# Kernel optimization log

Measured on AMD Instinct MI355X. Metric: run time of the kernel, lower is better.

## Reference

```python
import jax, jax.numpy as jnp
import numpy as np

B, T, D = 64, 512, 768
H1, H2, OUT = 512, 512, 256

def _masked_lstm(x, lengths, Wih, Whh, b):
    # x: [B,T,Din] -> (outs [B,T,H], final hidden [B,H]). torch gate order: i,f,g,o.
    Bm, Tm, _ = x.shape
    H = Whh.shape[1]
    x_proj = jnp.einsum('btd,gd->btg', x, Wih) + b          # [B,T,4H], input proj hoisted out of scan
    mask = jnp.arange(Tm)[None, :] < lengths[:, None]        # [B,T]
    def step(carry, inp):
        h, c = carry
        xg, m = inp
        gates = xg + h @ Whh.T
        i, f, g, o = jnp.split(gates, 4, axis=-1)
        c_new = jax.nn.sigmoid(f) * c + jax.nn.sigmoid(i) * jnp.tanh(g)
        h_new = jax.nn.sigmoid(o) * jnp.tanh(c_new)
        m = m[:, None]
        h = jnp.where(m, h_new, h)      # hold state past seq end (pack_padded semantics)
        c = jnp.where(m, c_new, c)
        return (h, c), jnp.where(m, h_new, 0.0)  # pad_packed zero-fills
    h0 = jnp.zeros((Bm, H), x.dtype)
    (hT, _), outs = jax.lax.scan(step, (h0, h0), (x_proj.transpose(1, 0, 2), mask.T))
    return outs.transpose(1, 0, 2), hT

def _reverse_valid(x, lengths):
    # reverse each row within its valid length; zeros beyond (packed-sequence reversal)
    Tm = x.shape[1]
    idx = lengths[:, None] - 1 - jnp.arange(Tm)[None, :]
    valid = idx >= 0
    xr = jnp.take_along_axis(x, jnp.clip(idx, 0, Tm - 1)[..., None], axis=1)
    return jnp.where(valid[..., None], xr, 0.0)

def _bilstm_sum(x, lengths, Wih_f, Whh_f, b_f, Wih_b, Whh_b, b_b):
    out_f, h_f = _masked_lstm(x, lengths, Wih_f, Whh_f, b_f)
    out_b_rev, h_b = _masked_lstm(_reverse_valid(x, lengths), lengths, Wih_b, Whh_b, b_b)
    return out_f + _reverse_valid(out_b_rev, lengths), h_f, h_b

def _forward(x, W1f_ih, W1f_hh, b1f, W1b_ih, W1b_hh, b1b,
             W2f_ih, W2f_hh, b2f, W2b_ih, W2b_hh, b2b, W3, b3):
    lengths = jnp.sum(x[:, :, 0] != 0, axis=1)               # pad_with = 0
    out1, _, _ = _bilstm_sum(x, lengths, W1f_ih, W1f_hh, b1f, W1b_ih, W1b_hh, b1b)
    # direction sum already done inside _bilstm_sum; dropout is identity at eval
    _, h2f, h2b = _bilstm_sum(out1, lengths, W2f_ih, W2f_hh, b2f, W2b_ih, W2b_hh, b2b)
    h = h2f + h2b                                             # out_h[-2] (fwd) + out_h[-1] (bwd)
    return h @ W3.T + b3

def setup_inputs() -> dict:
    key = jax.random.key(0)
    ks = jax.random.split(key, 16)
    lengths = jax.random.randint(ks[0], (B,), T // 2, T + 1)
    x = jax.random.normal(ks[1], (B, T, D), dtype=jnp.float32)
    x = x * (jnp.arange(T)[None, :] < lengths[:, None])[..., None].astype(jnp.float32)
    def w(k, shape, fan):
        return jax.random.uniform(k, shape, jnp.float32, -1.0, 1.0) / np.sqrt(fan).astype(np.float32)
    return {
        'x': x,
        'W1f_ih': w(ks[2], (4 * H1, D), H1), 'W1f_hh': w(ks[3], (4 * H1, H1), H1), 'b1f': w(ks[4], (4 * H1,), H1),
        'W1b_ih': w(ks[5], (4 * H1, D), H1), 'W1b_hh': w(ks[6], (4 * H1, H1), H1), 'b1b': w(ks[7], (4 * H1,), H1),
        'W2f_ih': w(ks[8], (4 * H2, H1), H2), 'W2f_hh': w(ks[9], (4 * H2, H2), H2), 'b2f': w(ks[10], (4 * H2,), H2),
        'W2b_ih': w(ks[11], (4 * H2, H1), H2), 'W2b_hh': w(ks[12], (4 * H2, H2), H2), 'b2b': w(ks[13], (4 * H2,), H2),
        'W3': w(ks[14], (OUT, H2), H2), 'b3': w(ks[15], (OUT,), H2),
    }

def reference(x, W1f_ih, W1f_hh, b1f, W1b_ih, W1b_hh, b1b,
              W2f_ih, W2f_hh, b2f, W2b_ih, W2b_hh, b2b, W3, b3):
    return _forward(x, W1f_ih, W1f_hh, b1f, W1b_ih, W1b_hh, b1b,
                    W2f_ih, W2f_hh, b2f, W2b_ih, W2b_hh, b2b, W3, b3)
```

## Files before the change

kernel.cpp:

```cpp
#include <hip/hip_runtime.h>


#define WS_B 64
#define WS_T 512
#define WS_D 768
#define WS_H 512
#define NTOK 32768

typedef unsigned short u16;
typedef unsigned int u32;
typedef __attribute__((ext_vector_type(8))) short short8;
typedef __attribute__((ext_vector_type(4))) float f32x4;

__device__ __forceinline__ float bf2f(u16 u) {
    u32 x = ((u32)u) << 16;
    return __builtin_bit_cast(float, x);
}
__device__ __forceinline__ u16 f2bf(float f) {
    u32 x = __builtin_bit_cast(u32, f);
    u32 r = (x + 0x7FFFu + ((x >> 16) & 1u)) >> 16;
    return (u16)r;
}
__device__ __forceinline__ float sigf(float x) {
    return __builtin_amdgcn_rcpf(1.0f + __builtin_amdgcn_exp2f(-1.4426950408889634f * x));
}
__device__ __forceinline__ float tanh_f(float x) {
    return 2.0f * __builtin_amdgcn_rcpf(1.0f + __builtin_amdgcn_exp2f(-2.8853900817779268f * x)) - 1.0f;
}
__device__ __forceinline__ void cstore_u16(u16* p, u16 v) {
    __hip_atomic_store(p, v, __ATOMIC_RELAXED, __HIP_MEMORY_SCOPE_AGENT);
}

__global__ void lengths_kernel(const float* __restrict__ x, int* __restrict__ len) {
    int b = blockIdx.x;
    float v = x[((size_t)b * WS_T + threadIdx.x) * WS_D];
    unsigned long long m = __ballot(v != 0.0f);
    __shared__ int part[8];
    if ((threadIdx.x & 63) == 0) part[threadIdx.x >> 6] = __popcll(m);
    __syncthreads();
    if (threadIdx.x == 0) {
        int s = 0;
        for (int i = 0; i < 8; ++i) s += part[i];
        len[b] = s;
    }
}

__global__ void cvt_kernel(const float* __restrict__ s, u16* __restrict__ d, int n4) {
    int i = blockIdx.x * 256 + threadIdx.x;
    if (i >= n4) return;
    float4 v = ((const float4*)s)[i];
    ushort4 r;
    r.x = f2bf(v.x); r.y = f2bf(v.y); r.z = f2bf(v.z); r.w = f2bf(v.w);
    ((ushort4*)d)[i] = r;
}

__global__ void add_bf16_kernel(u16* __restrict__ a, const u16* __restrict__ b, int n8) {
    int i = blockIdx.x * 256 + threadIdx.x;
    if (i >= n8) return;
    ushort4 va0 = ((const ushort4*)a)[2 * i], va1 = ((const ushort4*)a)[2 * i + 1];
    ushort4 vb0 = ((const ushort4*)b)[2 * i], vb1 = ((const ushort4*)b)[2 * i + 1];
    ushort4 r0, r1;
    r0.x = f2bf(bf2f(va0.x) + bf2f(vb0.x)); r0.y = f2bf(bf2f(va0.y) + bf2f(vb0.y));
    r0.z = f2bf(bf2f(va0.z) + bf2f(vb0.z)); r0.w = f2bf(bf2f(va0.w) + bf2f(vb0.w));
    r1.x = f2bf(bf2f(va1.x) + bf2f(vb1.x)); r1.y = f2bf(bf2f(va1.y) + bf2f(vb1.y));
    r1.z = f2bf(bf2f(va1.z) + bf2f(vb1.z)); r1.w = f2bf(bf2f(va1.w) + bf2f(vb1.w));
    ((ushort4*)a)[2 * i] = r0; ((ushort4*)a)[2 * i + 1] = r1;
}

#define BM 128
#define BN 128
#define BKT 64
template <int A32>
__global__ __launch_bounds__(256) void gemm_bt(
    const void* __restrict__ Av, const u16* __restrict__ W,
    const float* __restrict__ bias, _Float16* __restrict__ C,
    int M, int N, int K)
{
    __shared__ u16 As[BM * BKT];
    __shared__ u16 Bs[BN * BKT];
    const int tid = threadIdx.x;
    const int lane = tid & 63, w = tid >> 6;
    const int ntiles = N / BN;
    const int mt = blockIdx.x / ntiles, nt = blockIdx.x - mt * ntiles;
    const int m0 = mt * BM, n0 = nt * BN;
    const int wr = (w >> 1) * 64, wc = (w & 1) * 64;
    const int kin = (lane >> 4) << 4;
    f32x4 acc[4][4] = {};
    for (int k0 = 0; k0 < K; k0 += BKT) {
#pragma unroll
        for (int it = 0; it < 4; ++it) {
            int off = it * 4096 + tid * 16;
            int row = off >> 7;
            int ce = (off & 127) >> 1;
            const u16* gb = W + (size_t)(n0 + row) * K + (k0 + ce);
            char* lb = (char*)Bs + it * 4096 + w * 1024;
            __builtin_amdgcn_global_load_lds(
                (const __attribute__((address_space(1))) u32*)gb,
                (__attribute__((address_space(3))) u32*)lb, 16, 0, 0);
            if constexpr (A32) {
                const float* ga = (const float*)Av + (size_t)(m0 + row) * K + (k0 + ce);
                float4 v0 = ((const float4*)ga)[0];
                float4 v1 = ((const float4*)ga)[1];
                u32 p0 = ((u32)f2bf(v0.y) << 16) | f2bf(v0.x);
                u32 p1 = ((u32)f2bf(v0.w) << 16) | f2bf(v0.z);
                u32 p2 = ((u32)f2bf(v1.y) << 16) | f2bf(v1.x);
                u32 p3 = ((u32)f2bf(v1.w) << 16) | f2bf(v1.z);
                *(uint4*)((char*)As + off) = make_uint4(p0, p1, p2, p3);
            } else {
                const u16* ga = (const u16*)Av + (size_t)(m0 + row) * K + (k0 + ce);
                char* la = (char*)As + it * 4096 + w * 1024;
                __builtin_amdgcn_global_load_lds(
                    (const __attribute__((address_space(1))) u32*)ga,
                    (__attribute__((address_space(3))) u32*)la, 16, 0, 0);
            }
        }
        asm volatile("s_waitcnt vmcnt(0)" ::: "memory");
        __syncthreads();
#pragma unroll
        for (int ks = 0; ks < 2; ++ks) {
            short8 av[4], bv[4];
#pragma unroll
            for (int mi = 0; mi < 4; ++mi)
                av[mi] = *(const short8*)((const char*)As + (wr + mi * 16 + (lane & 15)) * 128 + ks * 64 + kin);
#pragma unroll
            for (int ni = 0; ni < 4; ++ni)
                bv[ni] = *(const short8*)((const char*)Bs + (wc + ni * 16 + (lane & 15)) * 128 + ks * 64 + kin);
#pragma unroll
            for (int mi = 0; mi < 4; ++mi)
#pragma unroll
                for (int ni = 0; ni < 4; ++ni)
                    acc[mi][ni] = __builtin_amdgcn_mfma_f32_16x16x32_bf16(av[mi], bv[ni], acc[mi][ni], 0, 0, 0);
        }
        __syncthreads();
    }
    const int crow0 = m0 + wr + ((lane >> 4) << 2);
    const int ccol0 = n0 + wc + (lane & 15);
#pragma unroll
    for (int ni = 0; ni < 4; ++ni) {
        float bs = bias[ccol0 + ni * 16];
#pragma unroll
        for (int mi = 0; mi < 4; ++mi)
#pragma unroll
            for (int e = 0; e < 4; ++e)
                C[(size_t)(crow0 + mi * 16 + e) * N + (ccol0 + ni * 16)] =
                    (_Float16)(acc[mi][ni][e] + bs);
    }
}

__global__ __launch_bounds__(256, 1) void lstm_rec(
    const u16* __restrict__ whhF, const u16* __restrict__ whhB,
    const _Float16* __restrict__ xgF, const _Float16* __restrict__ xgB,
    const int* __restrict__ lengths,
    u16* __restrict__ hb,
    float* __restrict__ hfin,
    u16* __restrict__ outF, u16* __restrict__ outB,
    int* __restrict__ flags,
    int writeOut, int dir0)
{
    __shared__ __align__(16) char wlds[65536];
    const int tid = threadIdx.x;
    const int lane = tid & 63, w = tid >> 6;
    const int grp = blockIdx.x >> 5, wgl = blockIdx.x & 31;
    const int dir = dir0 + grp;
    const int hb_col = wgl << 4;
    const u16* whh = dir ? whhB : whhF;
    const _Float16* xg = dir ? xgB : xgF;
    u16* outp = dir ? outB : outF;
    int* myflags = flags + (grp << 5);
    const int colL = lane & 15;
    const int hcol = hb_col + colL;
    const int qw = lane >> 4;
    const int arow = (w << 4) + colL;
    const int kofs = qw << 3;

#pragma unroll
    for (int j = 0; j < 16; ++j) {
        int f = (w << 4) + j, kk = f >> 2, g = f & 3;
        int R = (g << 9) + hb_col + colL;
        uint4 v = *(const uint4*)(whh + (size_t)R * WS_H + kk * 32 + kofs);
        *(uint4*)(wlds + f * 1024 + lane * 16) = v;
    }
    int mylen[4], myb[4];
#pragma unroll
    for (int e = 0; e < 4; ++e) {
        myb[e] = (w << 4) + (qw << 2) + e;
        mylen[e] = lengths[myb[e]];
    }
    float hreg[4] = {0.f, 0.f, 0.f, 0.f}, creg[4] = {0.f, 0.f, 0.f, 0.f};
    float xq[4][4];

#pragma unroll
    for (int e = 0; e < 4; ++e) {
        int len = mylen[e];
        int tx = dir ? (len - 1) : 0;
        int txc = tx < 0 ? 0 : (tx > 511 ? 511 : tx);
        const _Float16* xr = xg + ((size_t)(myb[e] * WS_T + txc) << 11);
        xq[e][0] = (float)xr[hcol];
        xq[e][1] = (float)xr[512 + hcol];
        xq[e][2] = (float)xr[1024 + hcol];
        xq[e][3] = (float)xr[1536 + hcol];
    }
    __syncthreads();

    for (int s = 0; s < WS_T; ++s) {
        const int pr = s & 1;
        const u16* hg = hb + (dir * 2 + pr) * 32768;
        u16* hw = hb + (dir * 2 + (pr ^ 1)) * 32768;

        short8 av[16];
#pragma unroll
        for (int kk = 0; kk < 16; ++kk)
            av[kk] = *(const short8*)(hg + arow * WS_H + kk * 32 + kofs);
        f32x4 acc[4] = {};
#pragma unroll
        for (int kk = 0; kk < 16; ++kk) {
            const char* wp = wlds + (kk << 12) + lane * 16;
#pragma unroll
            for (int g = 0; g < 4; ++g) {
                short8 bg = *(const short8*)(wp + (g << 10));
                acc[g] = __builtin_amdgcn_mfma_f32_16x16x32_bf16(av[kk], bg, acc[g], 0, 0, 0);
            }
        }

#pragma unroll
        for (int e = 0; e < 4; ++e) {
            if (s < mylen[e]) {
                float gi = acc[0][e] + xq[e][0];
                float gf = acc[1][e] + xq[e][1];
                float gg = acc[2][e] + xq[e][2];
                float go = acc[3][e] + xq[e][3];
                float cn = sigf(gf) * creg[e] + sigf(gi) * tanh_f(gg);
                creg[e] = cn;
                hreg[e] = sigf(go) * tanh_f(cn);
            }
            cstore_u16(hw + myb[e] * WS_H + hcol, f2bf(hreg[e]));
        }
        __syncthreads();
        if (tid == 0)
            __hip_atomic_store(&myflags[wgl], s + 1, __ATOMIC_RELAXED, __HIP_MEMORY_SCOPE_AGENT);

        if (writeOut) {
#pragma unroll
            for (int e = 0; e < 4; ++e) {
                int len = mylen[e];
                int tx = dir ? (len - 1 - s) : s;
                if (s < len)
                    outp[((size_t)(myb[e] * WS_T + tx)) * 512 + hcol] = f2bf(hreg[e]);
            }
        }
        if (s == WS_T - 1) {
#pragma unroll
            for (int e = 0; e < 4; ++e)
                hfin[dir * 32768 + myb[e] * WS_H + hcol] = hreg[e];
        }
        if (s < WS_T - 1) {
#pragma unroll
            for (int e = 0; e < 4; ++e) {
                int len = mylen[e];
                int tx = dir ? (len - 2 - s) : (s + 1);
                int txc = tx < 0 ? 0 : (tx > 511 ? 511 : tx);
                const _Float16* xr = xg + ((size_t)(myb[e] * WS_T + txc) << 11);
                xq[e][0] = (float)xr[hcol];
                xq[e][1] = (float)xr[512 + hcol];
                xq[e][2] = (float)xr[1024 + hcol];
                xq[e][3] = (float)xr[1536 + hcol];
            }
            if (tid < 32) {
                while (__hip_atomic_load(&myflags[tid], __ATOMIC_RELAXED, __HIP_MEMORY_SCOPE_AGENT) <= s)
                    __builtin_amdgcn_s_sleep(1);
            }
            __syncthreads();
            if (tid == 0) {
                int v = __hip_atomic_load(&myflags[0], __ATOMIC_ACQUIRE, __HIP_MEMORY_SCOPE_AGENT);
                asm volatile("" :: "v"(v));
            }
            __syncthreads();
        }
    }
}

__global__ void final_kernel(const float* __restrict__ hf, const float* __restrict__ hbk,
                             const float* __restrict__ W3, const float* __restrict__ b3,
                             float* __restrict__ out) {
    int b = blockIdx.x, o = threadIdx.x;
    __shared__ float h2[512];
    for (int k = threadIdx.x; k < 512; k += 256) h2[k] = hf[b * 512 + k] + hbk[b * 512 + k];
    __syncthreads();
    float s = b3[o];
#pragma unroll 8
    for (int k = 0; k < 512; ++k) s += h2[k] * W3[o * 512 + k];
    out[b * 256 + o] = s;
}

#define MB(x) ((size_t)(x) << 20)

extern "C" void kernel_launch(void* const* d_in, const int* in_sizes, int n_in,
                              void* d_out, int out_size, void* d_ws, size_t ws_size,
                              hipStream_t stream) {
    (void)in_sizes; (void)n_in; (void)out_size;
    const float* x      = (const float*)d_in[0];
    const float* b1f    = (const float*)d_in[3];
    const float* b1b    = (const float*)d_in[6];
    const float* b2f    = (const float*)d_in[9];
    const float* b2b    = (const float*)d_in[12];
    const float* W3     = (const float*)d_in[13];
    const float* b3     = (const float*)d_in[14];
    float* out = (float*)d_out;
    char* ws = (char*)d_ws;

    enum : size_t {
        O_LEN  = 0,
        O_FLG  = 512,
        O_HB1  = 4096,
        O_HB2  = O_HB1 + 262144,
        O_HF1  = O_HB2 + 262144,
        O_HF2  = O_HF1 + 262144,
        O_CTRL_END = O_HF2 + 262144
    };
    const size_t O_W1FH = MB(2),  O_W1BH = MB(4),  O_W2FH = MB(6),  O_W2BH = MB(8);
    const size_t O_W1FI = MB(10), O_W1BI = MB(13), O_W2FI = MB(16), O_W2BI = MB(18);
    const size_t O_OUTF = MB(20), O_OUTB = MB(52);
    const size_t O_XG0  = MB(84), O_XG1  = MB(212);
    const size_t NEED_SEQ = MB(212), NEED_PAR = MB(340);
    if (ws_size < NEED_SEQ) return;
    const bool par = ws_size >= NEED_PAR;

    (void)hipMemsetAsync(ws, 0, O_CTRL_END, stream);
    (void)hipMemsetAsync(ws + O_OUTF, 0, MB(64), stream);

    int* lenp = (int*)(ws + O_LEN);
    lengths_kernel<<<64, 512, 0, stream>>>(x, lenp);

    cvt_kernel<<<1024, 256, 0, stream>>>((const float*)d_in[2],  (u16*)(ws + O_W1FH), 262144);
    cvt_kernel<<<1024, 256, 0, stream>>>((const float*)d_in[5],  (u16*)(ws + O_W1BH), 262144);
    cvt_kernel<<<1024, 256, 0, stream>>>((const float*)d_in[8],  (u16*)(ws + O_W2FH), 262144);
    cvt_kernel<<<1024, 256, 0, stream>>>((const float*)d_in[11], (u16*)(ws + O_W2BH), 262144);
    cvt_kernel<<<1536, 256, 0, stream>>>((const float*)d_in[1],  (u16*)(ws + O_W1FI), 393216);
    cvt_kernel<<<1536, 256, 0, stream>>>((const float*)d_in[4],  (u16*)(ws + O_W1BI), 393216);
    cvt_kernel<<<1024, 256, 0, stream>>>((const float*)d_in[7],  (u16*)(ws + O_W2FI), 262144);
    cvt_kernel<<<1024, 256, 0, stream>>>((const float*)d_in[10], (u16*)(ws + O_W2BI), 262144);

    _Float16* xg0 = (_Float16*)(ws + O_XG0);
    _Float16* xg1 = par ? (_Float16*)(ws + O_XG1) : xg0;
    u16* outFp = (u16*)(ws + O_OUTF);
    u16* outBp = (u16*)(ws + O_OUTB);

    if (par) {
        gemm_bt<1><<<4096, 256, 0, stream>>>(x, (u16*)(ws + O_W1FI), b1f, xg0, NTOK, 2048, 768);
        gemm_bt<1><<<4096, 256, 0, stream>>>(x, (u16*)(ws + O_W1BI), b1b, xg1, NTOK, 2048, 768);
        lstm_rec<<<64, 256, 0, stream>>>((u16*)(ws + O_W1FH), (u16*)(ws + O_W1BH),
                                         xg0, xg1, lenp,
                                         (u16*)(ws + O_HB1), (float*)(ws + O_HF1),
                                         outFp, outBp, (int*)(ws + O_FLG), 1, 0);
        add_bf16_kernel<<<8192, 256, 0, stream>>>(outFp, outBp, 2097152);
        gemm_bt<0><<<4096, 256, 0, stream>>>(outFp, (u16*)(ws + O_W2FI), b2f, xg0, NTOK, 2048, 512);
        gemm_bt<0><<<4096, 256, 0, stream>>>(outFp, (u16*)(ws + O_W2BI), b2b, xg1, NTOK, 2048, 512);
        lstm_rec<<<64, 256, 0, stream>>>((u16*)(ws + O_W2FH), (u16*)(ws + O_W2BH),
                                         xg0, xg1, lenp,
                                         (u16*)(ws + O_HB2), (float*)(ws + O_HF2),
                                         outFp, outBp, (int*)(ws + O_FLG + 512), 0, 0);
    } else {
        gemm_bt<1><<<4096, 256, 0, stream>>>(x, (u16*)(ws + O_W1FI), b1f, xg0, NTOK, 2048, 768);
        lstm_rec<<<32, 256, 0, stream>>>((u16*)(ws + O_W1FH), (u16*)(ws + O_W1FH),
                                         xg0, xg0, lenp,
                                         (u16*)(ws + O_HB1), (float*)(ws + O_HF1),
                                         outFp, outBp, (int*)(ws + O_FLG), 1, 0);
        gemm_bt<1><<<4096, 256, 0, stream>>>(x, (u16*)(ws + O_W1BI), b1b, xg0, NTOK, 2048, 768);
        lstm_rec<<<32, 256, 0, stream>>>((u16*)(ws + O_W1BH), (u16*)(ws + O_W1BH),
                                         xg0, xg0, lenp,
                                         (u16*)(ws + O_HB1), (float*)(ws + O_HF1),
                                         outFp, outBp, (int*)(ws + O_FLG + 256), 1, 1);
        add_bf16_kernel<<<8192, 256, 0, stream>>>(outFp, outBp, 2097152);
        gemm_bt<0><<<4096, 256, 0, stream>>>(outFp, (u16*)(ws + O_W2FI), b2f, xg0, NTOK, 2048, 512);
        lstm_rec<<<32, 256, 0, stream>>>((u16*)(ws + O_W2FH), (u16*)(ws + O_W2FH),
                                         xg0, xg0, lenp,
                                         (u16*)(ws + O_HB2), (float*)(ws + O_HF2),
                                         outFp, outBp, (int*)(ws + O_FLG + 512), 0, 0);
        gemm_bt<0><<<4096, 256, 0, stream>>>(outFp, (u16*)(ws + O_W2BI), b2b, xg0, NTOK, 2048, 512);
        lstm_rec<<<32, 256, 0, stream>>>((u16*)(ws + O_W2BH), (u16*)(ws + O_W2BH),
                                         xg0, xg0, lenp,
                                         (u16*)(ws + O_HB2), (float*)(ws + O_HF2),
                                         outFp, outBp, (int*)(ws + O_FLG + 768), 0, 1);
    }
    final_kernel<<<64, 256, 0, stream>>>((const float*)(ws + O_HF2),
                                         (const float*)(ws + O_HF2) + 32768, W3, b3, out);
}
```

Baseline: 5.946 ms.

## Move inter-workgroup wait before h load and defer xq/output work past MFMA

Restructures the recurrent LSTM step loop: the spin-wait on peer workgroup flags moves to the top of each step, and the sleep is dropped in favour of a tight spin with an acquire fence. The next-step input projection loads and the previous step's output stores are issued right after the hidden-state loads, ahead of the MFMA chain, so their latency overlaps the matmul. The flag store becomes a release store, and one of the two extra __syncthreads per step is removed. The risk is more spin pressure on memory and reliance on correct release/acquire ordering between workgroups.

```diff
diff --git a/kernel.cpp b/kernel.cpp
--- a/kernel.cpp
+++ b/kernel.cpp
@@ -187,7 +187,7 @@
         mylen[e] = lengths[myb[e]];
     }
     float hreg[4] = {0.f, 0.f, 0.f, 0.f}, creg[4] = {0.f, 0.f, 0.f, 0.f};
-    float xq[4][4];
+    float xq[4][4], xqn[4][4];
 
 #pragma unroll
     for (int e = 0; e < 4; ++e) {
@@ -207,10 +207,45 @@
         const u16* hg = hb + (dir * 2 + pr) * 32768;
         u16* hw = hb + (dir * 2 + (pr ^ 1)) * 32768;
 
+        if (s) {
+            if (tid < 32) {
+                while (__hip_atomic_load(&myflags[tid], __ATOMIC_RELAXED,
+                                         __HIP_MEMORY_SCOPE_AGENT) < s) {}
+            }
+            __syncthreads();
+            __builtin_amdgcn_fence(__ATOMIC_ACQUIRE, "agent");
+        }
+
         short8 av[16];
 #pragma unroll
         for (int kk = 0; kk < 16; ++kk)
             av[kk] = *(const short8*)(hg + arow * WS_H + kk * 32 + kofs);
+        if (s < WS_T - 1) {
+#pragma unroll
+            for (int e = 0; e < 4; ++e) {
+                int len = mylen[e];
+                int tx = dir ? (len - 2 - s) : (s + 1);
+                int txc = tx < 0 ? 0 : (tx > 511 ? 511 : tx);
+                const _Float16* xr = xg + ((size_t)(myb[e] * WS_T + txc) << 11);
+                xqn[e][0] = (float)xr[hcol];
+                xqn[e][1] = (float)xr[512 + hcol];
+                xqn[e][2] = (float)xr[1024 + hcol];
+                xqn[e][3] = (float)xr[1536 + hcol];
+            }
+        }
+        if (writeOut && s) {
+#pragma unroll
+            for (int e = 0; e < 4; ++e) {
+                int len = mylen[e];
+                int t = s - 1;
+                if (t < len) {
+                    int tx = dir ? (len - 1 - t) : t;
+                    outp[((size_t)(myb[e] * WS_T + tx)) * 512 + hcol] = f2bf(hreg[e]);
+                }
+            }
+        }
+        __builtin_amdgcn_sched_barrier(0);
+
         f32x4 acc[4] = {};
 #pragma unroll
         for (int kk = 0; kk < 16; ++kk) {
@@ -237,46 +272,27 @@
         }
         __syncthreads();
         if (tid == 0)
-            __hip_atomic_store(&myflags[wgl], s + 1, __ATOMIC_RELAXED, __HIP_MEMORY_SCOPE_AGENT);
-
-        if (writeOut) {
-#pragma unroll
-            for (int e = 0; e < 4; ++e) {
-                int len = mylen[e];
-                int tx = dir ? (len - 1 - s) : s;
-                if (s < len)
-                    outp[((size_t)(myb[e] * WS_T + tx)) * 512 + hcol] = f2bf(hreg[e]);
-            }
-        }
-        if (s == WS_T - 1) {
-#pragma unroll
-            for (int e = 0; e < 4; ++e)
-                hfin[dir * 32768 + myb[e] * WS_H + hcol] = hreg[e];
-        }
-        if (s < WS_T - 1) {
-#pragma unroll
-            for (int e = 0; e < 4; ++e) {
-                int len = mylen[e];
-                int tx = dir ? (len - 2 - s) : (s + 1);
-                int txc = tx < 0 ? 0 : (tx > 511 ? 511 : tx);
-                const _Float16* xr = xg + ((size_t)(myb[e] * WS_T + txc) << 11);
-                xq[e][0] = (float)xr[hcol];
-                xq[e][1] = (float)xr[512 + hcol];
-                xq[e][2] = (float)xr[1024 + hcol];
-                xq[e][3] = (float)xr[1536 + hcol];
-            }
-            if (tid < 32) {
-                while (__hip_atomic_load(&myflags[tid], __ATOMIC_RELAXED, __HIP_MEMORY_SCOPE_AGENT) <= s)
-                    __builtin_amdgcn_s_sleep(1);
-            }
-            __syncthreads();
-            if (tid == 0) {
-                int v = __hip_atomic_load(&myflags[0], __ATOMIC_ACQUIRE, __HIP_MEMORY_SCOPE_AGENT);
-                asm volatile("" :: "v"(v));
-            }
-            __syncthreads();
-        }
-    }
+            __hip_atomic_store(&myflags[wgl], s + 1, __ATOMIC_RELEASE, __HIP_MEMORY_SCOPE_AGENT);
+#pragma unroll
+        for (int e = 0; e < 4; ++e) {
+            xq[e][0] = xqn[e][0]; xq[e][1] = xqn[e][1];
+            xq[e][2] = xqn[e][2]; xq[e][3] = xqn[e][3];
+        }
+    }
+
+    if (writeOut) {
+#pragma unroll
+        for (int e = 0; e < 4; ++e) {
+            int len = mylen[e];
+            if (WS_T - 1 < len) {
+                int tx = dir ? (len - WS_T) : (WS_T - 1);
+                outp[((size_t)(myb[e] * WS_T + tx)) * 512 + hcol] = f2bf(hreg[e]);
+            }
+        }
+    }
+#pragma unroll
+    for (int e = 0; e < 4; ++e)
+        hfin[dir * 32768 + myb[e] * WS_H + hcol] = hreg[e];
 }
 
 __global__ void final_kernel(const float* __restrict__ hf, const float* __restrict__ hbk,
```

Result: slower. 8.131 ms (+36.8%).
